# Kernel tuning notes

Measured on AMD Instinct MI355X. Metric: run time of the kernel, lower is better.

## Reference

```python
import jax, jax.numpy as jnp
import numpy as np

RANK = 16
ALPHA = 32
SCALING = ALPHA / RANK  # 2.0


def setup_inputs() -> dict:
    key = jax.random.key(0)
    k1, k2, k3 = jax.random.split(key, 3)
    B_, S, D, O = 2, 4096, 4096, 4096
    x = jax.random.normal(k1, (B_, S, D), dtype=jnp.float32)
    # Dequantized base weight, torch Linear layout [out, in]
    W_base = jax.random.normal(k2, (O, D), dtype=jnp.float32) * 0.02
    # kaiming_uniform-ish init for lora_A [rank, in]
    bound = float(np.sqrt(6.0 / (1 + 5) / D))
    A = jax.random.uniform(k3, (RANK, D), dtype=jnp.float32, minval=-bound, maxval=bound)
    # lora_B initialized to zeros [out, rank]
    Bm = jnp.zeros((O, RANK), dtype=jnp.float32)
    return {"x": x, "W_base": W_base, "A": A, "B": Bm}


def reference(x, W_base, A, B):
    # Y = x @ W_base^T + (x @ A^T) @ B^T * scaling   (dropout p=0 -> identity)
    base_out = jnp.einsum('bsd,od->bso', x, W_base)
    lora_mid = jnp.einsum('bsd,rd->bsr', x, A)        # [B,S,rank]
    lora_out = jnp.einsum('bsr,or->bso', lora_mid, B) # [B,S,out]
    return base_out + lora_out * SCALING
```

## Files before the change

kernel.cpp:

```cpp
#include <hip/hip_runtime.h>
#include <hip/hip_bf16.h>

typedef __attribute__((ext_vector_type(8))) __bf16 bf16x8;
typedef __attribute__((ext_vector_type(4))) float  f32x4;

__global__ __launch_bounds__(256) void cvt_f32_bf16(
    const float* __restrict__ in, __bf16* __restrict__ out, long n8)
{
    long i = (long)blockIdx.x * blockDim.x + threadIdx.x;
    long stride = (long)gridDim.x * blockDim.x;
    for (; i < n8; i += stride) {
        const f32x4* p = (const f32x4*)(in + i * 8);
        f32x4 a = p[0], b = p[1];
        bf16x8 o;
        o[0] = (__bf16)a[0]; o[1] = (__bf16)a[1];
        o[2] = (__bf16)a[2]; o[3] = (__bf16)a[3];
        o[4] = (__bf16)b[0]; o[5] = (__bf16)b[1];
        o[6] = (__bf16)b[2]; o[7] = (__bf16)b[3];
        *(bf16x8*)(out + i * 8) = o;
    }
}

__global__ __launch_bounds__(256) void mid_and_cvt(
    const float* __restrict__ x, const float* __restrict__ A,
    float* __restrict__ mid, __bf16* __restrict__ Xb, int K, int M)
{
    int tid = threadIdx.x;
    int m0 = blockIdx.x * 4;

    float acc[4][16];
#pragma unroll
    for (int row = 0; row < 4; ++row)
#pragma unroll
        for (int r = 0; r < 16; ++r) acc[row][r] = 0.f;

    int iters = K / 2048;
    for (int it = 0; it < iters; ++it) {
        int k = it * 2048 + tid * 8;
        f32x4 xv[4][2];
#pragma unroll
        for (int row = 0; row < 4; ++row) {
            if (m0 + row < M) {
                const float* xr = x + (size_t)(m0 + row) * K;
                xv[row][0] = *(const f32x4*)(xr + k);
                xv[row][1] = *(const f32x4*)(xr + k + 4);
            } else {
                f32x4 z = {0.f,0.f,0.f,0.f};
                xv[row][0] = z; xv[row][1] = z;
            }
            if (Xb && m0 + row < M) {
                bf16x8 o;
                o[0] = (__bf16)xv[row][0][0]; o[1] = (__bf16)xv[row][0][1];
                o[2] = (__bf16)xv[row][0][2]; o[3] = (__bf16)xv[row][0][3];
                o[4] = (__bf16)xv[row][1][0]; o[5] = (__bf16)xv[row][1][1];
                o[6] = (__bf16)xv[row][1][2]; o[7] = (__bf16)xv[row][1][3];
                *(bf16x8*)(Xb + (size_t)(m0 + row) * K + k) = o;
            }
        }
#pragma unroll
        for (int r = 0; r < 16; ++r) {
            const f32x4* ap = (const f32x4*)(A + (size_t)r * K + k);
            f32x4 a0 = ap[0], a1 = ap[1];
#pragma unroll
            for (int row = 0; row < 4; ++row) {
                acc[row][r] += xv[row][0][0]*a0[0] + xv[row][0][1]*a0[1]
                             + xv[row][0][2]*a0[2] + xv[row][0][3]*a0[3]
                             + xv[row][1][0]*a1[0] + xv[row][1][1]*a1[1]
                             + xv[row][1][2]*a1[2] + xv[row][1][3]*a1[3];
            }
        }
    }

#pragma unroll
    for (int row = 0; row < 4; ++row)
#pragma unroll
        for (int r = 0; r < 16; ++r)
#pragma unroll
            for (int off = 32; off > 0; off >>= 1)
                acc[row][r] += __shfl_down(acc[row][r], off, 64);

    __shared__ float red[4][4][16];
    int lane = tid & 63, w = tid >> 6;
    if (lane == 0) {
#pragma unroll
        for (int row = 0; row < 4; ++row)
#pragma unroll
            for (int r = 0; r < 16; ++r) red[w][row][r] = acc[row][r];
    }
    __syncthreads();
    if (tid < 64) {
        int row = tid >> 4, r = tid & 15;
        if (m0 + row < M) {
            float s = red[0][row][r] + red[1][row][r]
                    + red[2][row][r] + red[3][row][r];
            mid[(size_t)(m0 + row) * 16 + r] = s;
        }
    }
}

#define GL16(g, l) __builtin_amdgcn_global_load_lds( \
    (const __attribute__((address_space(1))) void*)(g), \
    (__attribute__((address_space(3))) void*)(l), 16, 0, 0)

#define LD8(base, off) (*(const bf16x8*)((const char*)(base) + (off)))

__global__ __launch_bounds__(512, 2) void gemm256(
    const __bf16* __restrict__ Xb,
    const __bf16* __restrict__ Wb,
    const float*  __restrict__ mid,
    const float*  __restrict__ Bl,
    float* __restrict__ out,
    int M, int N, int K)
{
    __shared__ __bf16 As[4][256 * 32];
    __shared__ __bf16 Bs[4][256 * 32];

    const int NT = K >> 5;

    int nbx = N >> 8, nby = M >> 8, nwg = nbx * nby;
    int bid = blockIdx.x, swz = bid;
    if ((nwg & 7) == 0) { int cpx = nwg >> 3; swz = (bid & 7) * cpx + (bid >> 3); }
    int by = swz / nbx, bx = swz % nbx;
    int m0 = by << 8, n0 = bx << 8;

    int tid = threadIdx.x;
    int lane = tid & 63;
    int w = tid >> 6;
    int wm = w >> 2, wn = w & 3;

    int q0 = tid >> 2;
    int c0 = tid & 3;
    int csrc = c0 ^ ((q0 >> 1) & 3);
    const __bf16* sA0 = Xb + (size_t)(m0 + q0) * K + csrc * 8;
    const __bf16* sA1 = sA0 + (size_t)128 * K;
    const __bf16* sB0 = Wb + (size_t)(n0 + q0) * K + csrc * 8;
    const __bf16* sB1 = sB0 + (size_t)128 * K;
    unsigned ldsw = (unsigned)w * 1024;

    int chunkSwz = (lane >> 4) ^ ((lane >> 1) & 3);
    unsigned aoff = (unsigned)((wm * 128 + (lane & 15)) * 64 + chunkSwz * 16);
    unsigned boff = (unsigned)((wn * 64  + (lane & 15)) * 64 + chunkSwz * 16);

#define STAGE_A(t, b) do { size_t ko = (size_t)(t) * 32; \
    GL16(sA0 + ko, (char*)As[b] + ldsw); \
    GL16(sA1 + ko, (char*)As[b] + 8192 + ldsw); } while (0)
#define STAGE_B(t, b) do { size_t ko = (size_t)(t) * 32; \
    GL16(sB0 + ko, (char*)Bs[b] + ldsw); \
    GL16(sB1 + ko, (char*)Bs[b] + 8192 + ldsw); } while (0)

    f32x4 acc[8][4];
    {
        int kh = lane >> 4;
        bf16x8 bI[4];
#pragma unroll
        for (int j = 0; j < 4; ++j) {
            bf16x8 v = {};
            if (kh < 2) {
                int col = n0 + wn * 64 + j * 16 + (lane & 15);
                const f32x4* p = (const f32x4*)(Bl + (size_t)col * 16 + kh * 8);
                f32x4 v0 = p[0], v1 = p[1];
                v[0] = (__bf16)(2.0f * v0[0]); v[1] = (__bf16)(2.0f * v0[1]);
                v[2] = (__bf16)(2.0f * v0[2]); v[3] = (__bf16)(2.0f * v0[3]);
                v[4] = (__bf16)(2.0f * v1[0]); v[5] = (__bf16)(2.0f * v1[1]);
                v[6] = (__bf16)(2.0f * v1[2]); v[7] = (__bf16)(2.0f * v1[3]);
            }
            bI[j] = v;
        }
#pragma unroll
        for (int i = 0; i < 8; ++i) {
            bf16x8 aI = {};
            if (kh < 2) {
                int row = m0 + wm * 128 + i * 16 + (lane & 15);
                const f32x4* p = (const f32x4*)(mid + (size_t)row * 16 + kh * 8);
                f32x4 v0 = p[0], v1 = p[1];
                aI[0] = (__bf16)v0[0]; aI[1] = (__bf16)v0[1];
                aI[2] = (__bf16)v0[2]; aI[3] = (__bf16)v0[3];
                aI[4] = (__bf16)v1[0]; aI[5] = (__bf16)v1[1];
                aI[6] = (__bf16)v1[2]; aI[7] = (__bf16)v1[3];
            }
            f32x4 z = {0.f, 0.f, 0.f, 0.f};
#pragma unroll
            for (int j = 0; j < 4; ++j)
                acc[i][j] = __builtin_amdgcn_mfma_f32_16x16x32_bf16(aI, bI[j], z, 0, 0, 0);
        }
    }

    STAGE_A(0, 0); STAGE_B(0, 0);
    STAGE_A(1, 1); STAGE_B(1, 1);
    asm volatile("s_waitcnt vmcnt(4)" ::: "memory");
    asm volatile("s_barrier" ::: "memory");

    bf16x8 axf0 = LD8(As[0], aoff);
    bf16x8 axf1 = LD8(As[0], aoff + 1024);
    bf16x8 axf2 = LD8(As[0], aoff + 2048);
    bf16x8 axf3 = LD8(As[0], aoff + 3072);
    bf16x8 bxf0 = LD8(Bs[0], boff);
    bf16x8 bxf1 = LD8(Bs[0], boff + 1024);
    bf16x8 bxf2 = LD8(Bs[0], boff + 2048);
    bf16x8 bxf3 = LD8(Bs[0], boff + 3072);

    for (int t = 0; t < NT; t += 2) {
        const char* cA0 = (const char*)As[t & 3];
        const char* cA1 = (const char*)As[(t + 1) & 3];
        const char* cB1 = (const char*)Bs[(t + 1) & 3];
        const char* cA2 = (const char*)As[(t + 2) & 3];
        const char* cB2 = (const char*)Bs[(t + 2) & 3];
        bool p2 = (t + 2) < NT;
        bool p3 = (t + 3) < NT;

        bf16x8 ax4 = LD8(cA0, aoff + 4096);
        bf16x8 ax5 = LD8(cA0, aoff + 5120);
        bf16x8 ax6 = LD8(cA0, aoff + 6144);
        bf16x8 ax7 = LD8(cA0, aoff + 7168);
        if (p2) STAGE_A(t + 2, (t + 2) & 3);
        asm volatile("s_barrier" ::: "memory");
        __builtin_amdgcn_s_setprio(1);
        acc[0][0] = __builtin_amdgcn_mfma_f32_16x16x32_bf16(axf0, bxf0, acc[0][0], 0, 0, 0);
        acc[0][1] = __builtin_amdgcn_mfma_f32_16x16x32_bf16(axf0, bxf1, acc[0][1], 0, 0, 0);
        acc[0][2] = __builtin_amdgcn_mfma_f32_16x16x32_bf16(axf0, bxf2, acc[0][2], 0, 0, 0);
        acc[0][3] = __builtin_amdgcn_mfma_f32_16x16x32_bf16(axf0, bxf3, acc[0][3], 0, 0, 0);
        acc[1][0] = __builtin_amdgcn_mfma_f32_16x16x32_bf16(axf1, bxf0, acc[1][0], 0, 0, 0);
        acc[1][1] = __builtin_amdgcn_mfma_f32_16x16x32_bf16(axf1, bxf1, acc[1][1], 0, 0, 0);
        acc[1][2] = __builtin_amdgcn_mfma_f32_16x16x32_bf16(axf1, bxf2, acc[1][2], 0, 0, 0);
        acc[1][3] = __builtin_amdgcn_mfma_f32_16x16x32_bf16(axf1, bxf3, acc[1][3], 0, 0, 0);
        acc[2][0] = __builtin_amdgcn_mfma_f32_16x16x32_bf16(axf2, bxf0, acc[2][0], 0, 0, 0);
        acc[2][1] = __builtin_amdgcn_mfma_f32_16x16x32_bf16(axf2, bxf1, acc[2][1], 0, 0, 0);
        acc[2][2] = __builtin_amdgcn_mfma_f32_16x16x32_bf16(axf2, bxf2, acc[2][2], 0, 0, 0);
        acc[2][3] = __builtin_amdgcn_mfma_f32_16x16x32_bf16(axf2, bxf3, acc[2][3], 0, 0, 0);
        acc[3][0] = __builtin_amdgcn_mfma_f32_16x16x32_bf16(axf3, bxf0, acc[3][0], 0, 0, 0);
        acc[3][1] = __builtin_amdgcn_mfma_f32_16x16x32_bf16(axf3, bxf1, acc[3][1], 0, 0, 0);
        acc[3][2] = __builtin_amdgcn_mfma_f32_16x16x32_bf16(axf3, bxf2, acc[3][2], 0, 0, 0);
        acc[3][3] = __builtin_amdgcn_mfma_f32_16x16x32_bf16(axf3, bxf3, acc[3][3], 0, 0, 0);
        __builtin_amdgcn_s_setprio(0);

        if (p2) STAGE_B(t + 2, (t + 2) & 3);
        if (p2) asm volatile("s_waitcnt vmcnt(4)" ::: "memory");
        else    asm volatile("s_waitcnt vmcnt(0)" ::: "memory");
        bf16x8 ayf0 = LD8(cA1, aoff);
        bf16x8 ayf1 = LD8(cA1, aoff + 1024);
        bf16x8 ayf2 = LD8(cA1, aoff + 2048);
        bf16x8 ayf3 = LD8(cA1, aoff + 3072);
        bf16x8 byf0 = LD8(cB1, boff);
        bf16x8 byf1 = LD8(cB1, boff + 1024);
        bf16x8 byf2 = LD8(cB1, boff + 2048);
        bf16x8 byf3 = LD8(cB1, boff + 3072);
        asm volatile("s_barrier" ::: "memory");
        __builtin_amdgcn_s_setprio(1);
        acc[4][0] = __builtin_amdgcn_mfma_f32_16x16x32_bf16(ax4, bxf0, acc[4][0], 0, 0, 0);
        acc[4][1] = __builtin_amdgcn_mfma_f32_16x16x32_bf16(ax4, bxf1, acc[4][1], 0, 0, 0);
        acc[4][2] = __builtin_amdgcn_mfma_f32_16x16x32_bf16(ax4, bxf2, acc[4][2], 0, 0, 0);
        acc[4][3] = __builtin_amdgcn_mfma_f32_16x16x32_bf16(ax4, bxf3, acc[4][3], 0, 0, 0);
        acc[5][0] = __builtin_amdgcn_mfma_f32_16x16x32_bf16(ax5, bxf0, acc[5][0], 0, 0, 0);
        acc[5][1] = __builtin_amdgcn_mfma_f32_16x16x32_bf16(ax5, bxf1, acc[5][1], 0, 0, 0);
        acc[5][2] = __builtin_amdgcn_mfma_f32_16x16x32_bf16(ax5, bxf2, acc[5][2], 0, 0, 0);
        acc[5][3] = __builtin_amdgcn_mfma_f32_16x16x32_bf16(ax5, bxf3, acc[5][3], 0, 0, 0);
        acc[6][0] = __builtin_amdgcn_mfma_f32_16x16x32_bf16(ax6, bxf0, acc[6][0], 0, 0, 0);
        acc[6][1] = __builtin_amdgcn_mfma_f32_16x16x32_bf16(ax6, bxf1, acc[6][1], 0, 0, 0);
        acc[6][2] = __builtin_amdgcn_mfma_f32_16x16x32_bf16(ax6, bxf2, acc[6][2], 0, 0, 0);
        acc[6][3] = __builtin_amdgcn_mfma_f32_16x16x32_bf16(ax6, bxf3, acc[6][3], 0, 0, 0);
        acc[7][0] = __builtin_amdgcn_mfma_f32_16x16x32_bf16(ax7, bxf0, acc[7][0], 0, 0, 0);
        acc[7][1] = __builtin_amdgcn_mfma_f32_16x16x32_bf16(ax7, bxf1, acc[7][1], 0, 0, 0);
        acc[7][2] = __builtin_amdgcn_mfma_f32_16x16x32_bf16(ax7, bxf2, acc[7][2], 0, 0, 0);
        acc[7][3] = __builtin_amdgcn_mfma_f32_16x16x32_bf16(ax7, bxf3, acc[7][3], 0, 0, 0);
        __builtin_amdgcn_s_setprio(0);

        bf16x8 ay4 = LD8(cA1, aoff + 4096);
        bf16x8 ay5 = LD8(cA1, aoff + 5120);
        bf16x8 ay6 = LD8(cA1, aoff + 6144);
        bf16x8 ay7 = LD8(cA1, aoff + 7168);
        if (p3) STAGE_A(t + 3, (t + 3) & 3);
        asm volatile("s_barrier" ::: "memory");
        __builtin_amdgcn_s_setprio(1);
        acc[0][0] = __builtin_amdgcn_mfma_f32_16x16x32_bf16(ayf0, byf0, acc[0][0], 0, 0, 0);
        acc[0][1] = __builtin_amdgcn_mfma_f32_16x16x32_bf16(ayf0, byf1, acc[0][1], 0, 0, 0);
        acc[0][2] = __builtin_amdgcn_mfma_f32_16x16x32_bf16(ayf0, byf2, acc[0][2], 0, 0, 0);
        acc[0][3] = __builtin_amdgcn_mfma_f32_16x16x32_bf16(ayf0, byf3, acc[0][3], 0, 0, 0);
        acc[1][0] = __builtin_amdgcn_mfma_f32_16x16x32_bf16(ayf1, byf0, acc[1][0], 0, 0, 0);
        acc[1][1] = __builtin_amdgcn_mfma_f32_16x16x32_bf16(ayf1, byf1, acc[1][1], 0, 0, 0);
        acc[1][2] = __builtin_amdgcn_mfma_f32_16x16x32_bf16(ayf1, byf2, acc[1][2], 0, 0, 0);
        acc[1][3] = __builtin_amdgcn_mfma_f32_16x16x32_bf16(ayf1, byf3, acc[1][3], 0, 0, 0);
        acc[2][0] = __builtin_amdgcn_mfma_f32_16x16x32_bf16(ayf2, byf0, acc[2][0], 0, 0, 0);
        acc[2][1] = __builtin_amdgcn_mfma_f32_16x16x32_bf16(ayf2, byf1, acc[2][1], 0, 0, 0);
        acc[2][2] = __builtin_amdgcn_mfma_f32_16x16x32_bf16(ayf2, byf2, acc[2][2], 0, 0, 0);
        acc[2][3] = __builtin_amdgcn_mfma_f32_16x16x32_bf16(ayf2, byf3, acc[2][3], 0, 0, 0);
        acc[3][0] = __builtin_amdgcn_mfma_f32_16x16x32_bf16(ayf3, byf0, acc[3][0], 0, 0, 0);
        acc[3][1] = __builtin_amdgcn_mfma_f32_16x16x32_bf16(ayf3, byf1, acc[3][1], 0, 0, 0);
        acc[3][2] = __builtin_amdgcn_mfma_f32_16x16x32_bf16(ayf3, byf2, acc[3][2], 0, 0, 0);
        acc[3][3] = __builtin_amdgcn_mfma_f32_16x16x32_bf16(ayf3, byf3, acc[3][3], 0, 0, 0);
        __builtin_amdgcn_s_setprio(0);

        if (p3) STAGE_B(t + 3, (t + 3) & 3);
        if (p3) asm volatile("s_waitcnt vmcnt(4)" ::: "memory");
        else    asm volatile("s_waitcnt vmcnt(0)" ::: "memory");
        if (p2) {
            axf0 = LD8(cA2, aoff);
            axf1 = LD8(cA2, aoff + 1024);
            axf2 = LD8(cA2, aoff + 2048);
            axf3 = LD8(cA2, aoff + 3072);
            bxf0 = LD8(cB2, boff);
            bxf1 = LD8(cB2, boff + 1024);
            bxf2 = LD8(cB2, boff + 2048);
            bxf3 = LD8(cB2, boff + 3072);
        }
        asm volatile("s_barrier" ::: "memory");
        __builtin_amdgcn_s_setprio(1);
        acc[4][0] = __builtin_amdgcn_mfma_f32_16x16x32_bf16(ay4, byf0, acc[4][0], 0, 0, 0);
        acc[4][1] = __builtin_amdgcn_mfma_f32_16x16x32_bf16(ay4, byf1, acc[4][1], 0, 0, 0);
        acc[4][2] = __builtin_amdgcn_mfma_f32_16x16x32_bf16(ay4, byf2, acc[4][2], 0, 0, 0);
        acc[4][3] = __builtin_amdgcn_mfma_f32_16x16x32_bf16(ay4, byf3, acc[4][3], 0, 0, 0);
        acc[5][0] = __builtin_amdgcn_mfma_f32_16x16x32_bf16(ay5, byf0, acc[5][0], 0, 0, 0);
        acc[5][1] = __builtin_amdgcn_mfma_f32_16x16x32_bf16(ay5, byf1, acc[5][1], 0, 0, 0);
        acc[5][2] = __builtin_amdgcn_mfma_f32_16x16x32_bf16(ay5, byf2, acc[5][2], 0, 0, 0);
        acc[5][3] = __builtin_amdgcn_mfma_f32_16x16x32_bf16(ay5, byf3, acc[5][3], 0, 0, 0);
        acc[6][0] = __builtin_amdgcn_mfma_f32_16x16x32_bf16(ay6, byf0, acc[6][0], 0, 0, 0);
        acc[6][1] = __builtin_amdgcn_mfma_f32_16x16x32_bf16(ay6, byf1, acc[6][1], 0, 0, 0);
        acc[6][2] = __builtin_amdgcn_mfma_f32_16x16x32_bf16(ay6, byf2, acc[6][2], 0, 0, 0);
        acc[6][3] = __builtin_amdgcn_mfma_f32_16x16x32_bf16(ay6, byf3, acc[6][3], 0, 0, 0);
        acc[7][0] = __builtin_amdgcn_mfma_f32_16x16x32_bf16(ay7, byf0, acc[7][0], 0, 0, 0);
        acc[7][1] = __builtin_amdgcn_mfma_f32_16x16x32_bf16(ay7, byf1, acc[7][1], 0, 0, 0);
        acc[7][2] = __builtin_amdgcn_mfma_f32_16x16x32_bf16(ay7, byf2, acc[7][2], 0, 0, 0);
        acc[7][3] = __builtin_amdgcn_mfma_f32_16x16x32_bf16(ay7, byf3, acc[7][3], 0, 0, 0);
        __builtin_amdgcn_s_setprio(0);
    }

#pragma unroll
    for (int i = 0; i < 8; ++i) {
        int rbase = m0 + wm * 128 + i * 16 + ((lane >> 4) << 2);
#pragma unroll
        for (int q = 0; q < 4; ++q) {
            float* orow = out + (size_t)(rbase + q) * N;
            int colb = n0 + wn * 64 + (lane & 15);
            orow[colb]      = acc[i][0][q];
            orow[colb + 16] = acc[i][1][q];
            orow[colb + 32] = acc[i][2][q];
            orow[colb + 48] = acc[i][3][q];
        }
    }
}

__global__ __launch_bounds__(256) void gemm_fb(
    const float* __restrict__ X, const float* __restrict__ W,
    const float* __restrict__ mid, const float* __restrict__ Bl,
    float* __restrict__ out, int M, int N, int K)
{
    __shared__ float As[64][16];
    __shared__ float Bs[64][16];
    int nbx = N / 64;
    int bx = blockIdx.x % nbx, by = blockIdx.x / nbx;
    int m0 = by * 64, n0 = bx * 64;
    int tid = threadIdx.x;
    int tr = tid >> 4, tc = tid & 15;

    float acc[4][4] = {};
    for (int kt = 0; kt < K; kt += 16) {
#pragma unroll
        for (int s = 0; s < 4; ++s) {
            int c = s * 256 + tid;
            int row = c >> 4, kk = c & 15;
            As[row][kk] = X[(size_t)(m0 + row) * K + kt + kk];
            Bs[row][kk] = W[(size_t)(n0 + row) * K + kt + kk];
        }
        __syncthreads();
#pragma unroll
        for (int kk = 0; kk < 16; ++kk) {
            float av[4], bv[4];
#pragma unroll
            for (int i = 0; i < 4; ++i) { av[i] = As[tr*4+i][kk]; bv[i] = Bs[tc*4+i][kk]; }
#pragma unroll
            for (int i = 0; i < 4; ++i)
#pragma unroll
                for (int j = 0; j < 4; ++j) acc[i][j] += av[i] * bv[j];
        }
        __syncthreads();
    }
#pragma unroll
    for (int i = 0; i < 4; ++i) {
        int row = m0 + tr * 4 + i;
#pragma unroll
        for (int j = 0; j < 4; ++j) {
            int col = n0 + tc * 4 + j;
            float s = 0.f;
#pragma unroll
            for (int r = 0; r < 16; ++r)
                s += mid[(size_t)row * 16 + r] * Bl[(size_t)col * 16 + r];
            out[(size_t)row * N + col] = acc[i][j] + 2.0f * s;
        }
    }
}

extern "C" void kernel_launch(void* const* d_in, const int* in_sizes, int n_in,
                              void* d_out, int out_size, void* d_ws, size_t ws_size,
                              hipStream_t stream)
{
    const float* x   = (const float*)d_in[0];
    const float* Wf  = (const float*)d_in[1];
    const float* A   = (const float*)d_in[2];
    const float* Bl  = (const float*)d_in[3];
    float* out = (float*)d_out;

    int D = in_sizes[2] / 16;
    int O = in_sizes[3] / 16;
    long M = (long)in_sizes[0] / D;
    int K = D, N = O;

    size_t xb_bytes  = (size_t)M * K * 2;
    size_t wb_bytes  = (size_t)N * K * 2;
    size_t mid_bytes = (size_t)M * 16 * 4;

    bool shapes_ok = (M % 256 == 0) && (N % 256 == 0) && (K % 2048 == 0);

    int midgrid = (int)((M + 3) / 4);

    if (shapes_ok && ws_size >= xb_bytes + wb_bytes + mid_bytes) {
        __bf16* Xb  = (__bf16*)d_ws;
        __bf16* Wbb = (__bf16*)((char*)d_ws + xb_bytes);
        float*  mid = (float*)((char*)d_ws + xb_bytes + wb_bytes);

        cvt_f32_bf16<<<2048, 256, 0, stream>>>(Wf, Wbb, (long)N * K / 8);
        mid_and_cvt<<<midgrid, 256, 0, stream>>>(x, A, mid, Xb, K, (int)M);
        int nwg = (int)(M / 256) * (N / 256);
        gemm256<<<nwg, 512, 0, stream>>>(Xb, Wbb, mid, Bl, out, (int)M, N, K);
    } else {
        float* mid = (float*)d_ws;
        mid_and_cvt<<<midgrid, 256, 0, stream>>>(x, A, mid, nullptr, K, (int)M);
        int nwg = (int)(M / 64) * (N / 64);
        gemm_fb<<<nwg, 256, 0, stream>>>(x, Wf, mid, Bl, out, (int)M, N, K);
    }
}
```

Baseline: 344.2 us.

## Issue LDS fragment reads via inline asm so they overlap the MFMA block

```diff
diff --git a/kernel.cpp b/kernel.cpp
--- a/kernel.cpp
+++ b/kernel.cpp
@@ -102,7 +102,12 @@
     (const __attribute__((address_space(1))) void*)(g), \
     (__attribute__((address_space(3))) void*)(l), 16, 0, 0)
 
-#define LD8(base, off) (*(const bf16x8*)((const char*)(base) + (off)))
+#define DSR(dst, addr, IMM) \
+    asm volatile("ds_read_b128 %0, %1 offset:" IMM : "=v"(dst) : "v"(addr))
+
+#define BAR()   __builtin_amdgcn_s_barrier()
+#define LGKM0() asm volatile("s_waitcnt lgkmcnt(0)" ::: )
+#define SCHED() __builtin_amdgcn_sched_barrier(0)
 
 __global__ __launch_bounds__(512, 2) void gemm256(
     const __bf16* __restrict__ Xb,
@@ -140,6 +145,9 @@
     int chunkSwz = (lane >> 4) ^ ((lane >> 1) & 3);
     unsigned aoff = (unsigned)((wm * 128 + (lane & 15)) * 64 + chunkSwz * 16);
     unsigned boff = (unsigned)((wn * 64  + (lane & 15)) * 64 + chunkSwz * 16);
+
+    unsigned a_addr = (unsigned)(size_t)(__attribute__((address_space(3))) __bf16*)&As[0][0] + aoff;
+    unsigned b_addr = (unsigned)(size_t)(__attribute__((address_space(3))) __bf16*)&Bs[0][0] + boff;
 
 #define STAGE_A(t, b) do { size_t ko = (size_t)(t) * 32; \
     GL16(sA0 + ko, (char*)As[b] + ldsw); \
@@ -188,32 +196,33 @@
     STAGE_A(0, 0); STAGE_B(0, 0);
     STAGE_A(1, 1); STAGE_B(1, 1);
     asm volatile("s_waitcnt vmcnt(4)" ::: "memory");
-    asm volatile("s_barrier" ::: "memory");
-
-    bf16x8 axf0 = LD8(As[0], aoff);
-    bf16x8 axf1 = LD8(As[0], aoff + 1024);
-    bf16x8 axf2 = LD8(As[0], aoff + 2048);
-    bf16x8 axf3 = LD8(As[0], aoff + 3072);
-    bf16x8 bxf0 = LD8(Bs[0], boff);
-    bf16x8 bxf1 = LD8(Bs[0], boff + 1024);
-    bf16x8 bxf2 = LD8(Bs[0], boff + 2048);
-    bf16x8 bxf3 = LD8(Bs[0], boff + 3072);
+    BAR();
+
+    bf16x8 axf0, axf1, axf2, axf3, bxf0, bxf1, bxf2, bxf3;
+    bf16x8 ayf0, ayf1, ayf2, ayf3, byf0, byf1, byf2, byf3;
+    bf16x8 ax4, ax5, ax6, ax7, ay4, ay5, ay6, ay7;
+
+    DSR(axf0, a_addr, "0");    DSR(axf1, a_addr, "1024");
+    DSR(axf2, a_addr, "2048"); DSR(axf3, a_addr, "3072");
+    DSR(bxf0, b_addr, "0");    DSR(bxf1, b_addr, "1024");
+    DSR(bxf2, b_addr, "2048"); DSR(bxf3, b_addr, "3072");
 
     for (int t = 0; t < NT; t += 2) {
-        const char* cA0 = (const char*)As[t & 3];
-        const char* cA1 = (const char*)As[(t + 1) & 3];
-        const char* cB1 = (const char*)Bs[(t + 1) & 3];
-        const char* cA2 = (const char*)As[(t + 2) & 3];
-        const char* cB2 = (const char*)Bs[(t + 2) & 3];
+        unsigned aT0 = a_addr + ((unsigned)(t & 3) << 14);
+        unsigned aT1 = a_addr + ((unsigned)((t + 1) & 3) << 14);
+        unsigned bT1 = b_addr + ((unsigned)((t + 1) & 3) << 14);
+        unsigned aT2 = a_addr + ((unsigned)((t + 2) & 3) << 14);
+        unsigned bT2 = b_addr + ((unsigned)((t + 2) & 3) << 14);
         bool p2 = (t + 2) < NT;
         bool p3 = (t + 3) < NT;
 
-        bf16x8 ax4 = LD8(cA0, aoff + 4096);
-        bf16x8 ax5 = LD8(cA0, aoff + 5120);
-        bf16x8 ax6 = LD8(cA0, aoff + 6144);
-        bf16x8 ax7 = LD8(cA0, aoff + 7168);
         if (p2) STAGE_A(t + 2, (t + 2) & 3);
-        asm volatile("s_barrier" ::: "memory");
+        BAR();
+        LGKM0();
+        SCHED();
+        DSR(ax4, aT0, "4096"); DSR(ax5, aT0, "5120");
+        DSR(ax6, aT0, "6144"); DSR(ax7, aT0, "7168");
+        SCHED();
         __builtin_amdgcn_s_setprio(1);
         acc[0][0] = __builtin_amdgcn_mfma_f32_16x16x32_bf16(axf0, bxf0, acc[0][0], 0, 0, 0);
         acc[0][1] = __builtin_amdgcn_mfma_f32_16x16x32_bf16(axf0, bxf1, acc[0][1], 0, 0, 0);
@@ -233,18 +242,20 @@
         acc[3][3] = __builtin_amdgcn_mfma_f32_16x16x32_bf16(axf3, bxf3, acc[3][3], 0, 0, 0);
         __builtin_amdgcn_s_setprio(0);
 
-        if (p2) STAGE_B(t + 2, (t + 2) & 3);
-        if (p2) asm volatile("s_waitcnt vmcnt(4)" ::: "memory");
-        else    asm volatile("s_waitcnt vmcnt(0)" ::: "memory");
-        bf16x8 ayf0 = LD8(cA1, aoff);
-        bf16x8 ayf1 = LD8(cA1, aoff + 1024);
-        bf16x8 ayf2 = LD8(cA1, aoff + 2048);
-        bf16x8 ayf3 = LD8(cA1, aoff + 3072);
-        bf16x8 byf0 = LD8(cB1, boff);
-        bf16x8 byf1 = LD8(cB1, boff + 1024);
-        bf16x8 byf2 = LD8(cB1, boff + 2048);
-        bf16x8 byf3 = LD8(cB1, boff + 3072);
-        asm volatile("s_barrier" ::: "memory");
+        if (p2) {
+            STAGE_B(t + 2, (t + 2) & 3);
+            asm volatile("s_waitcnt vmcnt(4)" ::: "memory");
+        } else {
+            asm volatile("s_waitcnt vmcnt(0)" ::: "memory");
+        }
+        BAR();
+        LGKM0();
+        SCHED();
+        DSR(ayf0, aT1, "0");    DSR(ayf1, aT1, "1024");
+        DSR(ayf2, aT1, "2048"); DSR(ayf3, aT1, "3072");
+        DSR(byf0, bT1, "0");    DSR(byf1, bT1, "1024");
+        DSR(byf2, bT1, "2048"); DSR(byf3, bT1, "3072");
+        SCHED();
         __builtin_amdgcn_s_setprio(1);
         acc[4][0] = __builtin_amdgcn_mfma_f32_16x16x32_bf16(ax4, bxf0, acc[4][0], 0, 0, 0);
         acc[4][1] = __builtin_amdgcn_mfma_f32_16x16x32_bf16(ax4, bxf1, acc[4][1], 0, 0, 0);
@@ -264,12 +275,13 @@
         acc[7][3] = __builtin_amdgcn_mfma_f32_16x16x32_bf16(ax7, bxf3, acc[7][3], 0, 0, 0);
         __builtin_amdgcn_s_setprio(0);
 
-        bf16x8 ay4 = LD8(cA1, aoff + 4096);
-        bf16x8 ay5 = LD8(cA1, aoff + 5120);
-        bf16x8 ay6 = LD8(cA1, aoff + 6144);
-        bf16x8 ay7 = LD8(cA1, aoff + 7168);
         if (p3) STAGE_A(t + 3, (t + 3) & 3);
-        asm volatile("s_barrier" ::: "memory");
+        BAR();
+        LGKM0();
+        SCHED();
+        DSR(ay4, aT1, "4096"); DSR(ay5, aT1, "5120");
+        DSR(ay6, aT1, "6144"); DSR(ay7, aT1, "7168");
+        SCHED();
         __builtin_amdgcn_s_setprio(1);
         acc[0][0] = __builtin_amdgcn_mfma_f32_16x16x32_bf16(ayf0, byf0, acc[0][0], 0, 0, 0);
         acc[0][1] = __builtin_amdgcn_mfma_f32_16x16x32_bf16(ayf0, byf1, acc[0][1], 0, 0, 0);
@@ -289,20 +301,22 @@
         acc[3][3] = __builtin_amdgcn_mfma_f32_16x16x32_bf16(ayf3, byf3, acc[3][3], 0, 0, 0);
         __builtin_amdgcn_s_setprio(0);
 
-        if (p3) STAGE_B(t + 3, (t + 3) & 3);
-        if (p3) asm volatile("s_waitcnt vmcnt(4)" ::: "memory");
-        else    asm volatile("s_waitcnt vmcnt(0)" ::: "memory");
+        if (p3) {
+            STAGE_B(t + 3, (t + 3) & 3);
+            asm volatile("s_waitcnt vmcnt(4)" ::: "memory");
+        } else {
+            asm volatile("s_waitcnt vmcnt(0)" ::: "memory");
+        }
+        BAR();
+        LGKM0();
+        SCHED();
         if (p2) {
-            axf0 = LD8(cA2, aoff);
-            axf1 = LD8(cA2, aoff + 1024);
-            axf2 = LD8(cA2, aoff + 2048);
-            axf3 = LD8(cA2, aoff + 3072);
-            bxf0 = LD8(cB2, boff);
-            bxf1 = LD8(cB2, boff + 1024);
-            bxf2 = LD8(cB2, boff + 2048);
-            bxf3 = LD8(cB2, boff + 3072);
-        }
-        asm volatile("s_barrier" ::: "memory");
+            DSR(axf0, aT2, "0");    DSR(axf1, aT2, "1024");
+            DSR(axf2, aT2, "2048"); DSR(axf3, aT2, "3072");
+            DSR(bxf0, bT2, "0");    DSR(bxf1, bT2, "1024");
+            DSR(bxf2, bT2, "2048"); DSR(bxf3, bT2, "3072");
+        }
+        SCHED();
         __builtin_amdgcn_s_setprio(1);
         acc[4][0] = __builtin_amdgcn_mfma_f32_16x16x32_bf16(ay4, byf0, acc[4][0], 0, 0, 0);
         acc[4][1] = __builtin_amdgcn_mfma_f32_16x16x32_bf16(ay4, byf1, acc[4][1], 0, 0, 0);
```

Measured after the change: 331.6 us. 3.7% less time.
